# Optimization experiments

Hardware: AMD Instinct MI355X
Metric: run time of the kernel (lower is better)

## Reference

```python
import jax, jax.numpy as jnp
from jax import lax
import numpy as np

E = 256        # encoded_part_size
H = 1500       # builder_hidden_dim == construction_plan_size
QIN = 2 * E    # query_in_size
Q1, Q = 600, 300
EV1, EV2, EV3, EV4 = 1000, 100, 10, 1
B, N = 32, 32  # batch, parts


def _lin(key, fan_in, shape):
    b = 1.0 / np.sqrt(fan_in)
    return jax.random.uniform(key, shape, jnp.float32, -b, b)


def setup_inputs() -> dict:
    key = jax.random.key(0)
    ks = jax.random.split(key, 20)
    inp = {"x": jax.random.normal(ks[0], (B, N, E), jnp.float32)}
    # LSTMCell params (torch gate order i,f,g,o)
    inp["w_ih"] = _lin(ks[1], H, (4 * H, E))
    inp["w_hh"] = _lin(ks[2], H, (4 * H, H))
    inp["b_ih"] = _lin(ks[3], H, (4 * H,))
    inp["b_hh"] = _lin(ks[4], H, (4 * H,))
    # query MLP
    inp["q1_w"] = _lin(ks[5], QIN, (Q1, QIN)); inp["q1_b"] = _lin(ks[6], QIN, (Q1,))
    inp["q2_w"] = _lin(ks[7], Q1, (Q, Q1));   inp["q2_b"] = _lin(ks[8], Q1, (Q,))
    # evaluator MLP
    inp["e1_w"] = _lin(ks[9], H + Q, (EV1, H + Q)); inp["e1_b"] = _lin(ks[10], H + Q, (EV1,))
    inp["e2_w"] = _lin(ks[11], EV1, (EV2, EV1));    inp["e2_b"] = _lin(ks[12], EV1, (EV2,))
    inp["e3_w"] = _lin(ks[13], EV2, (EV3, EV2));    inp["e3_b"] = _lin(ks[14], EV2, (EV3,))
    inp["e4_w"] = _lin(ks[15], EV3, (EV4, EV3));    inp["e4_b"] = _lin(ks[16], EV3, (EV4,))
    return inp


def reference(x, w_ih, w_hh, b_ih, b_hh, q1_w, q1_b, q2_w, q2_b,
              e1_w, e1_b, e2_w, e2_b, e3_w, e3_b, e4_w, e4_b):
    b, n, e = x.shape
    h = w_hh.shape[1]

    # ---- makeConstructionPlan: sort parts, run LSTMCell over the sequence ----
    seq = jnp.sort(x, axis=1).transpose(1, 0, 2)  # [n, B, E]

    def step(carry, xt):
        hs, cs = carry
        g = xt @ w_ih.T + b_ih + hs @ w_hh.T + b_hh  # [B, 4H]
        gi, gf, gg, go = jnp.split(g, 4, axis=-1)
        cs = jax.nn.sigmoid(gf) * cs + jax.nn.sigmoid(gi) * jnp.tanh(gg)
        hs = jax.nn.sigmoid(go) * jnp.tanh(cs)
        return (hs, cs), None

    z = jnp.zeros((b, h), x.dtype)
    (plan, _), _ = lax.scan(step, (z, z), seq)  # plan: [B, H]

    # ---- all pairs (i<j), batched instead of O(n^2) Python loop ----
    ii, jj = jnp.triu_indices(n, k=1)                       # P pairs, row-major order
    pairs = jnp.concatenate([x[:, ii], x[:, jj]], axis=-1)  # [B, P, 2E]

    # PositionalEncoding at position 0: sin(0)=0 on even dims, cos(0)=1 on odd dims
    pe = jnp.zeros((2 * e,), x.dtype).at[1::2].set(1.0)
    q = jax.nn.relu((pairs + pe) @ q1_w.T + q1_b)
    q = jax.nn.relu(q @ q2_w.T + q2_b)                      # [B, P, Qs]

    # evaluator: split the concat GEMM so the [B,P,H+Q] concat is never materialized
    ev = jax.nn.relu((plan @ e1_w[:, :h].T + e1_b)[:, None, :] + q @ e1_w[:, h:].T)
    ev = jax.nn.relu(ev @ e2_w.T + e2_b)
    ev = jax.nn.relu(ev @ e3_w.T + e3_b)
    ev = jax.nn.relu(ev @ e4_w.T + e4_b)                    # [B, P, 1]
    return ev[..., 0]                                       # [B, P]
```

## Files before the change

kernel.cpp:

```cpp
#include <hip/hip_runtime.h>
#include <math.h>

#define BB 32
#define NN 32
#define EE 256
#define HH 1500
#define G4 6000
#define QIN 512
#define Q1O 600
#define QO 300
#define EV1 1000
#define EV2 100
#define EV3 10
#define PP 496
#define ROWS (BB*PP)
#define BH (BB*HH)

#define TROW 40
#define TPLANE (128 * TROW)

#define LKT 47
#define LBLK 375
#define LTILE 1024
#define HSZ (LKT * LTILE)
#define LTILE_W 512
#define HSZW (LKT * LTILE_W)

typedef __attribute__((ext_vector_type(8))) short bf16x8;
typedef __attribute__((ext_vector_type(4))) float f32x4;

__device__ __forceinline__ float sigm(float x) { return 1.f / (1.f + expf(-x)); }

__device__ __forceinline__ unsigned bf16h(float x) {
    unsigned u = __float_as_uint(x);
    return (u + 0x7FFFu + ((u >> 16) & 1u)) & 0xFFFF0000u;
}

__device__ __forceinline__ void split4(float4 v, short* hp, short* lp) {
    unsigned h0 = bf16h(v.x), h1 = bf16h(v.y), h2 = bf16h(v.z), h3 = bf16h(v.w);
    float r0 = v.x - __uint_as_float(h0);
    float r1 = v.y - __uint_as_float(h1);
    float r2 = v.z - __uint_as_float(h2);
    float r3 = v.w - __uint_as_float(h3);
    unsigned l0 = bf16h(r0), l1 = bf16h(r1), l2 = bf16h(r2), l3 = bf16h(r3);
    uint2 hw, lw;
    hw.x = (h0 >> 16) | (h1 & 0xFFFF0000u);
    hw.y = (h2 >> 16) | (h3 & 0xFFFF0000u);
    lw.x = (l0 >> 16) | (l1 & 0xFFFF0000u);
    lw.y = (l2 >> 16) | (l3 & 0xFFFF0000u);
    *(uint2*)hp = hw;
    *(uint2*)lp = lw;
}

__device__ __forceinline__ void hi4(float4 v, short* hp) {
    unsigned h0 = bf16h(v.x), h1 = bf16h(v.y), h2 = bf16h(v.z), h3 = bf16h(v.w);
    uint2 hw;
    hw.x = (h0 >> 16) | (h1 & 0xFFFF0000u);
    hw.y = (h2 >> 16) | (h3 & 0xFFFF0000u);
    *(uint2*)hp = hw;
}

#define ASYNC16(dst, src) \
    __builtin_amdgcn_global_load_lds((const __attribute__((address_space(1))) unsigned*)(src), \
                                     (__attribute__((address_space(3))) unsigned*)(dst), 16, 0, 0)

__global__ void k_zero(float* a, int n) {
    int i = blockIdx.x * 256 + threadIdx.x;
    if (i < n) a[i] = 0.f;
}

__global__ void k_iijj(int* iijj) {
    int p = threadIdx.x;
    if (p >= PP) return;
    int i = 0, p0 = 0;
    while (p >= p0 + (NN - 1 - i)) { p0 += NN - 1 - i; i++; }
    iijj[p] = i;
    iijj[PP + p] = i + 1 + (p - p0);
}

__global__ void k_q1beff(const float* q1w, const float* q1b, float* beff) {
    int o = blockIdx.x * 256 + threadIdx.x;
    if (o >= Q1O) return;
    float a = q1b[o];
    for (int k = 1; k < QIN; k += 2) a += q1w[o * QIN + k];
    beff[o] = a;
}

__global__ void k_addb(const float* a, const float* b, float* c, int n) {
    int i = blockIdx.x * 256 + threadIdx.x;
    if (i < n) c[i] = a[i] + b[i];
}

__global__ void k_transpose(const float* __restrict__ src, float* __restrict__ dst,
                            int R, int C, int c0, int csub) {
    __shared__ float tile[32][33];
    int cb = blockIdx.x * 32, rb = blockIdx.y * 32;
    for (int dy = threadIdx.y; dy < 32; dy += 8) {
        int r = rb + dy, c = cb + threadIdx.x;
        if (r < R && c < csub) tile[dy][threadIdx.x] = src[(size_t)r * C + c0 + c];
    }
    __syncthreads();
    for (int dy = threadIdx.y; dy < 32; dy += 8) {
        int c = cb + dy, r = rb + threadIdx.x;
        if (c < csub && r < R) dst[(size_t)c * R + r] = tile[threadIdx.x][dy];
    }
}

__global__ void k_pack(const float* __restrict__ src, int ld, int col0, int NR, int K,
                       short* __restrict__ D) {
    int kt = blockIdx.x, mt = blockIdx.y, KT = gridDim.x;
    size_t tb = ((size_t)mt * KT + kt) * (2 * TPLANE);
    for (int idx = threadIdx.x; idx < 1024; idx += 256) {
        int rowin = idx >> 3, k4 = (idx & 7) << 2;
        int r = mt * 128 + rowin, k = kt * 32 + k4;
        float4 v = {0.f, 0.f, 0.f, 0.f};
        if (r < NR && k < K) v = *(const float4*)(src + (size_t)r * ld + col0 + k);
        size_t o = tb + rowin * TROW + k4;
        split4(v, D + o, D + o + TPLANE);
    }
}

__global__ void k_pack1(const float* __restrict__ src, int ld, int col0, int NR, int K,
                        short* __restrict__ D) {
    int kt = blockIdx.x, mt = blockIdx.y, KT = gridDim.x;
    size_t tb = ((size_t)mt * KT + kt) * TPLANE;
    for (int idx = threadIdx.x; idx < 1024; idx += 256) {
        int rowin = idx >> 3, k4 = (idx & 7) << 2;
        int r = mt * 128 + rowin, k = kt * 32 + k4;
        float4 v = {0.f, 0.f, 0.f, 0.f};
        if (r < NR && k < K) v = *(const float4*)(src + (size_t)r * ld + col0 + k);
        hi4(v, D + tb + rowin * TROW + k4);
    }
}

__global__ void k_pack_wf(const float* __restrict__ whh, short* __restrict__ wf) {
    int kt = blockIdx.x, blk = blockIdx.y;
    size_t tb = ((size_t)blk * LKT + kt) * LTILE_W;
    int t = threadIdx.x;
    int row = t >> 3, k4 = (t & 7) << 2;
    int g = row & 3, h_glob = blk * 4 + (row >> 2);
    int k = kt * 32 + k4;
    float4 v = {0.f, 0.f, 0.f, 0.f};
    if (k < HH) {
        int j = g * HH + h_glob;
        v = *(const float4*)(whh + (size_t)j * HH + k);
    }
    hi4(v, wf + tb + row * 32 + k4);
}

__global__ void k_sort(const float* __restrict__ x, float* __restrict__ seq) {
    int tid = blockIdx.x * 256 + threadIdx.x;
    if (tid >= BB * EE) return;
    int b = tid / EE, e = tid % EE;
    float v[NN];
#pragma unroll
    for (int n = 0; n < NN; n++) v[n] = x[(b * NN + n) * EE + e];
#pragma unroll
    for (int kk = 2; kk <= NN; kk <<= 1) {
#pragma unroll
        for (int jj = kk >> 1; jj > 0; jj >>= 1) {
#pragma unroll
            for (int i = 0; i < NN; i++) {
                int l = i ^ jj;
                if (l > i) {
                    bool up = (i & kk) == 0;
                    float a = v[i], c = v[l];
                    bool sw = up ? (a > c) : (a < c);
                    float lo = sw ? c : a, hi = sw ? a : c;
                    v[i] = lo; v[l] = hi;
                }
            }
        }
    }
#pragma unroll
    for (int n = 0; n < NN; n++) seq[(n * BB + b) * EE + e] = v[n];
}

__global__ void k_pairs(const float* __restrict__ x, const int* __restrict__ iijj,
                        short* __restrict__ P) {
    int idx = blockIdx.x * 256 + threadIdx.x;
    int r = idx >> 7;
    if (r >= ROWS) return;
    int q = idx & 127, k = q << 2;
    int b = r / PP, p = r - b * PP;
    int part = (k < EE) ? iijj[p] : iijj[PP + p];
    float4 v = *(const float4*)(x + (size_t)(b * NN + part) * EE + (k & (EE - 1)));
    int mt = r >> 7, rowin = r & 127, kt = k >> 5, k4 = k & 31;
    size_t o = ((size_t)mt * 16 + kt) * TPLANE + rowin * TROW + k4;
    hi4(v, P + o);
}

template<int APL, int BPL, int PPL>
__global__ __launch_bounds__(256, 2)
void k_gemm_t(const short* __restrict__ Ap, int AKT, const short* __restrict__ Bp,
              const float* __restrict__ bias, const float* __restrict__ pbm,
              float* __restrict__ Cf32, short* __restrict__ P, int PKT,
              int M, int K, int N, int relu, int cmode) {
    const int ATS = APL * TPLANE;
    const int BTS = BPL * TPLANE;
    constexpr bool PIPE = (APL == 1 && BPL == 1);
    constexpr int DEPTH = PIPE ? 3 : 2;
    __shared__ __align__(16) short lds[DEPTH][(APL + BPL) * TPLANE];

    int MT = M >> 7, NT = (N + 127) >> 7;
    int bid = blockIdx.x;
    int xcd = bid & 7, rr = bid >> 3;
    int nt = rr % NT, mtc = rr / NT;
    int mt = mtc * 8 + xcd;
    if (mt >= MT) return;

    int tid = threadIdx.x;
    int lane = tid & 63, w = tid >> 6;
    int wr = w >> 1, wc = w & 1;
    int ksteps = (K + 31) >> 5;

    const short* gA = Ap + (size_t)mt * AKT * ATS;
    const short* gB = Bp + (size_t)nt * ksteps * BTS;

    f32x4 acc[4][4];
#pragma unroll
    for (int mi = 0; mi < 4; mi++)
#pragma unroll
        for (int ni = 0; ni < 4; ni++) acc[mi][ni] = (f32x4){0.f, 0.f, 0.f, 0.f};

    int l15 = lane & 15;
    int kc8 = (lane >> 4) << 3;

    if constexpr (PIPE) {
#define STAGE3(bufi, kt) do { \
            _Pragma("unroll") \
            for (int i_ = 0; i_ < 5; i_++) { \
                int c_ = w * 5 + i_; \
                const short* s_ = (c_ < 10) \
                    ? gA + (size_t)(kt) * ATS + (c_ << 9) + lane * 8 \
                    : gB + (size_t)(kt) * BTS + ((c_ - 10) << 9) + lane * 8; \
                ASYNC16(&lds[bufi][c_ << 9], s_); \
            } \
        } while (0)

        STAGE3(0, 0);
        if (ksteps > 1) STAGE3(1, 1);

        int cbuf = 0, sbuf = 2;
        for (int kt = 0; kt < ksteps; kt++) {
            if (kt + 1 < ksteps) asm volatile("s_waitcnt vmcnt(5)" ::: "memory");
            else                 asm volatile("s_waitcnt vmcnt(0)" ::: "memory");
            __builtin_amdgcn_s_barrier();

            const short* LA = &lds[cbuf][0];
            const short* LB = &lds[cbuf][TPLANE];
            bf16x8 ah[4];
#pragma unroll
            for (int mi = 0; mi < 4; mi++)
                ah[mi] = *(const bf16x8*)(LA + (wr * 64 + mi * 16 + l15) * TROW + kc8);
#pragma unroll
            for (int ni = 0; ni < 4; ni++) {
                bf16x8 bh = *(const bf16x8*)(LB + (wc * 64 + ni * 16 + l15) * TROW + kc8);
#pragma unroll
                for (int mi = 0; mi < 4; mi++)
                    acc[mi][ni] = __builtin_amdgcn_mfma_f32_16x16x32_bf16(ah[mi], bh, acc[mi][ni], 0, 0, 0);
            }
            if (kt + 2 < ksteps) STAGE3(sbuf, kt + 2);
            cbuf = (cbuf == 2) ? 0 : cbuf + 1;
            sbuf = (sbuf == 2) ? 0 : sbuf + 1;
        }
#undef STAGE3
    } else {
#define STAGE(bufi, kt) do { \
            const short* sa_ = gA + (size_t)(kt) * ATS + lane * 8; \
            const short* sb_ = gB + (size_t)(kt) * BTS + lane * 8; \
            for (int c_ = w; c_ < ATS / 512; c_ += 4) \
                ASYNC16(&lds[bufi][c_ * 512], sa_ + c_ * 512); \
            for (int c_ = w; c_ < BTS / 512; c_ += 4) \
                ASYNC16(&lds[bufi][ATS + c_ * 512], sb_ + c_ * 512); \
        } while (0)

        STAGE(0, 0);
        __syncthreads();
        int buf = 0;
        for (int kt = 0; kt < ksteps; kt++) {
            if (kt + 1 < ksteps) STAGE(buf ^ 1, kt + 1);
            const short* LA = &lds[buf][0];
            const short* LB = &lds[buf][ATS];
            bf16x8 ah[4], al[4];
#pragma unroll
            for (int mi = 0; mi < 4; mi++) {
                int o = (wr * 64 + mi * 16 + l15) * TROW + kc8;
                ah[mi] = *(const bf16x8*)(LA + o);
                if constexpr (APL == 2) al[mi] = *(const bf16x8*)(LA + TPLANE + o);
            }
#pragma unroll
            for (int ni = 0; ni < 4; ni++) {
                int o = (wc * 64 + ni * 16 + l15) * TROW + kc8;
                bf16x8 bh = *(const bf16x8*)(LB + o);
                bf16x8 bl;
                if constexpr (BPL == 2) bl = *(const bf16x8*)(LB + TPLANE + o);
#pragma unroll
                for (int mi = 0; mi < 4; mi++) {
                    acc[mi][ni] = __builtin_amdgcn_mfma_f32_16x16x32_bf16(ah[mi], bh, acc[mi][ni], 0, 0, 0);
                    if constexpr (BPL == 2)
                        acc[mi][ni] = __builtin_amdgcn_mfma_f32_16x16x32_bf16(ah[mi], bl, acc[mi][ni], 0, 0, 0);
                    if constexpr (APL == 2)
                        acc[mi][ni] = __builtin_amdgcn_mfma_f32_16x16x32_bf16(al[mi], bh, acc[mi][ni], 0, 0, 0);
                }
            }
            __syncthreads();
            buf ^= 1;
        }
#undef STAGE
    }

    const int PTS = PPL * TPLANE;
#pragma unroll
    for (int ni = 0; ni < 4; ni++) {
        int col = nt * 128 + wc * 64 + ni * 16 + l15;
        float bb = (cmode == 0 && bias && col < N) ? bias[col] : 0.f;
#pragma unroll
        for (int mi = 0; mi < 4; mi++) {
            int rbase = mt * 128 + wr * 64 + mi * 16 + ((lane >> 4) << 2);
#pragma unroll
            for (int r4 = 0; r4 < 4; r4++) {
                int row = rbase + r4;
                float v = acc[mi][ni][r4];
                if (cmode == 1) {
                    if (row < G4)
                        Cf32[(size_t)(col >> 5) * (G4 * BB) + (size_t)row * BB + (col & 31)]
                            = v + bias[row];
                    continue;
                }
                v += bb;
                if (pbm && col < N) v += pbm[(size_t)(row / PP) * N + col];
                if (relu) v = fmaxf(v, 0.f);
                if (Cf32 && col < N) Cf32[(size_t)row * N + col] = v;
                if (P) {
                    unsigned h = bf16h(v);
                    int kt2 = col >> 5, kin = col & 31, rowin = row & 127, mtt = row >> 7;
                    size_t o = ((size_t)mtt * PKT + kt2) * PTS + rowin * TROW + kin;
                    P[o] = (short)(h >> 16);
                    if constexpr (PPL == 2) {
                        unsigned l = bf16h(v - __uint_as_float(h));
                        P[o + TPLANE] = (short)(l >> 16);
                    }
                }
            }
        }
    }
}

__global__ __launch_bounds__(512, 1)
void k_lstm_step(const short* __restrict__ wf, const short* __restrict__ hbuf_r,
                 short* __restrict__ hbuf_w, const float* __restrict__ xgT_n,
                 float* __restrict__ ct, float* __restrict__ ht, int writeht) {
    __shared__ f32x4 red[3][2][64];
    int tid = threadIdx.x, lane = tid & 63, wave = tid >> 6;
    int ks = wave >> 1, mi = wave & 1;
    int blk = blockIdx.x;
    int l15 = lane & 15, bg = lane >> 4;
    int kc8 = bg << 3;
    int n = l15, g = n & 3;
    int h_glob = blk * 4 + (n >> 2);
    int kt0 = ks * 12, ktend = (ks == 3) ? LKT : (kt0 + 12);

    f32x4 acc = {0.f, 0.f, 0.f, 0.f};
    if (ks == 0)
        acc = *(const f32x4*)(xgT_n + (size_t)(g * HH + h_glob) * BB + mi * 16 + bg * 4);

    const short* wp0 = wf + (size_t)blk * HSZW + l15 * 32 + kc8;
    const short* hp0 = hbuf_r + (mi * 16 + l15) * 32 + kc8;

    bf16x8 a0 = *(const bf16x8*)(hp0 + (size_t)kt0 * LTILE);
    bf16x8 b0 = *(const bf16x8*)(wp0 + (size_t)kt0 * LTILE_W);
    bf16x8 a1 = *(const bf16x8*)(hp0 + (size_t)(kt0 + 1) * LTILE);
    bf16x8 b1 = *(const bf16x8*)(wp0 + (size_t)(kt0 + 1) * LTILE_W);
    bf16x8 a2 = *(const bf16x8*)(hp0 + (size_t)(kt0 + 2) * LTILE);
    bf16x8 b2 = *(const bf16x8*)(wp0 + (size_t)(kt0 + 2) * LTILE_W);
    for (int kt = kt0; kt < ktend; kt++) {
        bf16x8 a3, b3;
        if (kt + 3 < ktend) {
            a3 = *(const bf16x8*)(hp0 + (size_t)(kt + 3) * LTILE);
            b3 = *(const bf16x8*)(wp0 + (size_t)(kt + 3) * LTILE_W);
        }
        acc = __builtin_amdgcn_mfma_f32_16x16x32_bf16(a0, b0, acc, 0, 0, 0);
        a0 = a1; b0 = b1;
        a1 = a2; b1 = b2;
        a2 = a3; b2 = b3;
    }

    if (ks > 0) red[ks - 1][mi][lane] = acc;
    __syncthreads();
    if (ks > 0) return;
    acc += red[0][mi][lane] + red[1][mi][lane] + red[2][mi][lane];

    float gg[4][4];
#pragma unroll
    for (int r = 0; r < 4; r++) {
        float a = acc[r];
        gg[0][r] = a;
        gg[1][r] = __shfl_xor(a, 1);
        gg[2][r] = __shfl_xor(a, 2);
        gg[3][r] = __shfl_xor(a, 3);
    }

    if ((n & 3) == 0) {
        int kth = h_glob >> 5, kin = h_glob & 31;
#pragma unroll
        for (int r = 0; r < 4; r++) {
            int b = mi * 16 + bg * 4 + r;
            float ci = ct[h_glob * BB + b];
            float cn = sigm(gg[1][r]) * ci + sigm(gg[0][r]) * tanhf(gg[2][r]);
            ct[h_glob * BB + b] = cn;
            float hv = sigm(gg[3][r]) * tanhf(cn);
            if (writeht) ht[h_glob * BB + b] = hv;
            unsigned hh = bf16h(hv);
            size_t o = (size_t)kth * LTILE + b * 32 + kin;
            __builtin_nontemporal_store((short)(hh >> 16), &hbuf_w[o]);
        }
    }
}

__global__ void k_pb(const float* __restrict__ ht, const float* __restrict__ e1at,
                     const float* __restrict__ e1b, float* __restrict__ pb) {
    __shared__ float ps[HH];
    int b = blockIdx.y;
    for (int idx = threadIdx.x; idx < HH; idx += 256) ps[idx] = ht[(size_t)idx * BB + b];
    __syncthreads();
    int o = blockIdx.x * 256 + threadIdx.x;
    if (o >= EV1) return;
    float acc = e1b[o];
    for (int k = 0; k < HH; k++) acc += ps[k] * e1at[(size_t)k * EV1 + o];
    pb[b * EV1 + o] = acc;
}

__global__ void k_e34(const float* __restrict__ e2out, const float* __restrict__ e3t,
                      const float* __restrict__ e3b, const float* __restrict__ e4w,
                      const float* __restrict__ e4b, float* __restrict__ out) {
    __shared__ float wt[EV2 * EV3];
    for (int idx = threadIdx.x; idx < EV2 * EV3; idx += 256) wt[idx] = e3t[idx];
    __syncthreads();
    int r = blockIdx.x * 256 + threadIdx.x;
    if (r >= ROWS) return;
    float h3[EV3];
#pragma unroll
    for (int o3 = 0; o3 < EV3; o3++) h3[o3] = e3b[o3];
    for (int k = 0; k < EV2; k++) {
        float v = e2out[(size_t)r * EV2 + k];
#pragma unroll
        for (int o3 = 0; o3 < EV3; o3++) h3[o3] += v * wt[k * EV3 + o3];
    }
    float acc = e4b[0];
#pragma unroll
    for (int o3 = 0; o3 < EV3; o3++) acc += fmaxf(h3[o3], 0.f) * e4w[o3];
    out[r] = fmaxf(acc, 0.f);
}

extern "C" void kernel_launch(void* const* d_in, const int* in_sizes, int n_in,
                              void* d_out, int out_size, void* d_ws, size_t ws_size,
                              hipStream_t stream) {
    const float* x    = (const float*)d_in[0];
    const float* w_ih = (const float*)d_in[1];
    const float* w_hh = (const float*)d_in[2];
    const float* b_ih = (const float*)d_in[3];
    const float* b_hh = (const float*)d_in[4];
    const float* q1_w = (const float*)d_in[5];
    const float* q1_b = (const float*)d_in[6];
    const float* q2_w = (const float*)d_in[7];
    const float* q2_b = (const float*)d_in[8];
    const float* e1_w = (const float*)d_in[9];
    const float* e1_b = (const float*)d_in[10];
    const float* e2_w = (const float*)d_in[11];
    const float* e2_b = (const float*)d_in[12];
    const float* e3_w = (const float*)d_in[13];
    const float* e3_b = (const float*)d_in[14];
    const float* e4_w = (const float*)d_in[15];
    const float* e4_b = (const float*)d_in[16];
    float* out = (float*)d_out;
    float* ws = (float*)d_ws;

    size_t off = 0;
    float* seq    = ws + off; off += (size_t)NN * BB * EE;
    size_t regionA = off; off += 23000000;
    short* wf       = (short*)(ws + regionA);
    short* seq_p    = (short*)(ws + regionA + 4600000);
    short* wih_p    = (short*)(ws + regionA + 5000000);
    short* pairs_p  = (short*)(ws + regionA);
    short* q1out_p  = (short*)(ws + regionA + 10200000);
    short* e1out_p  = (short*)(ws + regionA);
    float* e2out    = ws + regionA + 20400000;
    float* xgT    = ws + off; off += 7618560;
    short* q2out_p  = (short*)xgT;
    float* ht     = ws + off; off += BH;
    float* ct     = ws + off; off += BH;
    short* hbuf   = (short*)(ws + off); off += 48128;
    short* q1w_p  = (short*)(ws + off); off += 409600;
    short* q2w_p  = (short*)(ws + off); off += 291840;
    short* e1w_p  = (short*)(ws + off); off += 409600;
    short* e2w_p  = (short*)(ws + off); off += 163840;
    float* e1at   = ws + off; off += (size_t)HH * EV1;
    float* e3t    = ws + off; off += 1024;
    float* pb     = ws + off; off += BB * EV1;
    float* q1beff = ws + off; off += 1024;
    float* bsum   = ws + off; off += 6016;
    int*   iijj   = (int*)(ws + off); off += 1024;

    dim3 tb(32, 8);

    k_iijj<<<1, 512, 0, stream>>>(iijj);
    k_q1beff<<<3, 256, 0, stream>>>(q1_w, q1_b, q1beff);
    k_addb<<<24, 256, 0, stream>>>(b_ih, b_hh, bsum, G4);
    k_zero<<<376, 256, 0, stream>>>(ct, BH + 48128);

    k_pack_wf<<<dim3(LKT, LBLK), 128, 0, stream>>>(w_hh, wf);
    k_transpose<<<dim3(47, 32), tb, 0, stream>>>(e1_w, e1at, EV1, HH + QO, 0, HH);
    k_transpose<<<dim3(4, 1), tb, 0, stream>>>(e3_w, e3t, EV3, EV2, 0, EV2);
    k_pack<<<dim3(8, 47), 256, 0, stream>>>(w_ih, EE, 0, G4, EE, wih_p);
    k_pack1<<<dim3(16, 5), 256, 0, stream>>>(q1_w, QIN, 0, Q1O, QIN, q1w_p);
    k_pack1<<<dim3(19, 3), 256, 0, stream>>>(q2_w, Q1O, 0, QO, Q1O, q2w_p);
    k_pack1<<<dim3(10, 8), 256, 0, stream>>>(e1_w, HH + QO, HH, EV1, QO, e1w_p);
    k_pack1<<<dim3(32, 1), 256, 0, stream>>>(e2_w, EV1, 0, EV2, EV1, e2w_p);

    k_sort<<<32, 256, 0, stream>>>(x, seq);
    k_pack<<<dim3(8, 8), 256, 0, stream>>>(seq, EE, 0, 1024, EE, seq_p);
    k_gemm_t<2, 2, 1><<<8 * 8 * 6, 256, 0, stream>>>(wih_p, 8, seq_p, bsum, nullptr,
                                                     xgT, nullptr, 0, 6016, EE, 1024, 0, 1);

    for (int nstep = 0; nstep < NN; nstep++) {
        const short* hr = hbuf + (size_t)(nstep & 1) * HSZ;
        short* hw = hbuf + (size_t)((nstep + 1) & 1) * HSZ;
        k_lstm_step<<<LBLK, 512, 0, stream>>>(wf, hr, hw,
                                              xgT + (size_t)nstep * (G4 * BB), ct, ht,
                                              nstep == NN - 1);
    }

    k_pb<<<dim3(4, BB), 256, 0, stream>>>(ht, e1at, e1_b, pb);

    k_pairs<<<7936, 256, 0, stream>>>(x, iijj, pairs_p);
    k_gemm_t<1, 1, 1><<<8 * 5 * 16, 256, 0, stream>>>(pairs_p, 16, q1w_p, q1beff, nullptr,
                                                      nullptr, q1out_p, 20, ROWS, QIN, Q1O, 1, 0);
    k_gemm_t<1, 1, 1><<<8 * 3 * 16, 256, 0, stream>>>(q1out_p, 20, q2w_p, q2_b, nullptr,
                                                      nullptr, q2out_p, 12, ROWS, Q1O, QO, 1, 0);
    k_gemm_t<1, 1, 1><<<8 * 8 * 16, 256, 0, stream>>>(q2out_p, 12, e1w_p, nullptr, pb,
                                                      nullptr, e1out_p, 32, ROWS, QO, EV1, 1, 0);
    k_gemm_t<1, 1, 1><<<8 * 1 * 16, 256, 0, stream>>>(e1out_p, 32, e2w_p, e2_b, nullptr,
                                                      e2out, nullptr, 0, ROWS, EV1, EV2, 1, 0);
    k_e34<<<62, 256, 0, stream>>>(e2out, e3t, e3_b, e4_w, e4_b, out);
}
```

Baseline: 766.7 us.

## Deepen GEMM async pipeline to four stages and stage bf16 epilogue through LDS

The pipelined GEMM now uses four LDS buffers with three k-tiles prefetched, and the vmcnt waits are adjusted to how many loads are still in flight. The packed-bf16 output epilogue is also rewritten for the pipelined variant. It writes results into LDS tiles, loads the per-batch bias rows once into LDS, and copies whole tiles to global memory with 16-byte stores instead of scattered 2-byte stores. The cost is more LDS per block, which may lower occupancy under launch_bounds(256,2), plus extra barriers in the epilogue.

```diff
diff --git a/kernel.cpp b/kernel.cpp
--- a/kernel.cpp
+++ b/kernel.cpp
@@ -199,7 +199,7 @@
     const int ATS = APL * TPLANE;
     const int BTS = BPL * TPLANE;
     constexpr bool PIPE = (APL == 1 && BPL == 1);
-    constexpr int DEPTH = PIPE ? 3 : 2;
+    constexpr int DEPTH = PIPE ? 4 : 2;
     __shared__ __align__(16) short lds[DEPTH][(APL + BPL) * TPLANE];
 
     int MT = M >> 7, NT = (N + 127) >> 7;
@@ -240,15 +240,17 @@
 
         STAGE3(0, 0);
         if (ksteps > 1) STAGE3(1, 1);
-
-        int cbuf = 0, sbuf = 2;
+        if (ksteps > 2) STAGE3(2, 2);
+
         for (int kt = 0; kt < ksteps; kt++) {
-            if (kt + 1 < ksteps) asm volatile("s_waitcnt vmcnt(5)" ::: "memory");
+            int ahead = ksteps - 1 - kt;
+            if (ahead >= 2)      asm volatile("s_waitcnt vmcnt(10)" ::: "memory");
+            else if (ahead == 1) asm volatile("s_waitcnt vmcnt(5)" ::: "memory");
             else                 asm volatile("s_waitcnt vmcnt(0)" ::: "memory");
             __builtin_amdgcn_s_barrier();
 
-            const short* LA = &lds[cbuf][0];
-            const short* LB = &lds[cbuf][TPLANE];
+            const short* LA = &lds[kt & 3][0];
+            const short* LB = &lds[kt & 3][TPLANE];
             bf16x8 ah[4];
 #pragma unroll
             for (int mi = 0; mi < 4; mi++)
@@ -260,9 +262,7 @@
                 for (int mi = 0; mi < 4; mi++)
                     acc[mi][ni] = __builtin_amdgcn_mfma_f32_16x16x32_bf16(ah[mi], bh, acc[mi][ni], 0, 0, 0);
             }
-            if (kt + 2 < ksteps) STAGE3(sbuf, kt + 2);
-            cbuf = (cbuf == 2) ? 0 : cbuf + 1;
-            sbuf = (sbuf == 2) ? 0 : sbuf + 1;
+            if (kt + 3 < ksteps) STAGE3((kt + 3) & 3, kt + 3);
         }
 #undef STAGE3
     } else {
@@ -310,36 +310,90 @@
 #undef STAGE
     }
 
-    const int PTS = PPL * TPLANE;
-#pragma unroll
-    for (int ni = 0; ni < 4; ni++) {
-        int col = nt * 128 + wc * 64 + ni * 16 + l15;
-        float bb = (cmode == 0 && bias && col < N) ? bias[col] : 0.f;
-#pragma unroll
-        for (int mi = 0; mi < 4; mi++) {
-            int rbase = mt * 128 + wr * 64 + mi * 16 + ((lane >> 4) << 2);
-#pragma unroll
-            for (int r4 = 0; r4 < 4; r4++) {
-                int row = rbase + r4;
-                float v = acc[mi][ni][r4];
-                if (cmode == 1) {
-                    if (row < G4)
-                        Cf32[(size_t)(col >> 5) * (G4 * BB) + (size_t)row * BB + (col & 31)]
-                            = v + bias[row];
-                    continue;
+    bool done = false;
+    if constexpr (PIPE) {
+        if (P) {
+            short* obuf = &lds[0][0];
+            float* pbv  = (float*)&lds[1][0];
+            int b0 = (mt * 128) / PP;
+            int thr = (b0 + 1) * PP;
+            __syncthreads();
+            if (pbm) {
+                int c = nt * 128 + (tid & 127);
+                int bsel = (tid < 128) ? b0 : min(b0 + 1, BB - 1);
+                pbv[tid] = (c < N) ? pbm[(size_t)bsel * N + c] : 0.f;
+            }
+            __syncthreads();
+            int bg = lane >> 4;
+#pragma unroll
+            for (int r = 0; r < 2; r++) {
+#pragma unroll
+                for (int p = 0; p < 2; p++) {
+                    int ni = 2 * r + p;
+                    int col = nt * 128 + wc * 64 + ni * 16 + l15;
+                    int colloc = wc * 64 + ni * 16 + l15;
+                    float bb = (bias && col < N) ? bias[col] : 0.f;
+                    int kin = p * 16 + l15;
+#pragma unroll
+                    for (int mi = 0; mi < 4; mi++) {
+#pragma unroll
+                        for (int r4 = 0; r4 < 4; r4++) {
+                            int rowin = wr * 64 + mi * 16 + (bg << 2) + r4;
+                            float v = acc[mi][ni][r4] + bb;
+                            if (pbm) {
+                                int row = mt * 128 + rowin;
+                                v += pbv[(row >= thr ? 128 : 0) + colloc];
+                            }
+                            if (relu) v = fmaxf(v, 0.f);
+                            obuf[wc * 5120 + rowin * 40 + kin] = (short)(bf16h(v) >> 16);
+                        }
+                    }
                 }
-                v += bb;
-                if (pbm && col < N) v += pbm[(size_t)(row / PP) * N + col];
-                if (relu) v = fmaxf(v, 0.f);
-                if (Cf32 && col < N) Cf32[(size_t)row * N + col] = v;
-                if (P) {
-                    unsigned h = bf16h(v);
-                    int kt2 = col >> 5, kin = col & 31, rowin = row & 127, mtt = row >> 7;
-                    size_t o = ((size_t)mtt * PKT + kt2) * PTS + rowin * TROW + kin;
-                    P[o] = (short)(h >> 16);
-                    if constexpr (PPL == 2) {
-                        unsigned l = bf16h(v - __uint_as_float(h));
-                        P[o + TPLANE] = (short)(l >> 16);
+                __syncthreads();
+#pragma unroll
+                for (int reg = 0; reg < 2; reg++) {
+                    int ktg = nt * 4 + reg * 2 + r;
+                    uint4* dst = (uint4*)(P + ((size_t)mt * PKT + ktg) * TPLANE);
+                    const uint4* srcl = (const uint4*)(obuf + reg * 5120);
+                    for (int c = tid; c < 640; c += 256) dst[c] = srcl[c];
+                }
+                __syncthreads();
+            }
+            done = true;
+        }
+    }
+    if (!done) {
+        const int PTS = PPL * TPLANE;
+#pragma unroll
+        for (int ni = 0; ni < 4; ni++) {
+            int col = nt * 128 + wc * 64 + ni * 16 + l15;
+            float bb = (cmode == 0 && bias && col < N) ? bias[col] : 0.f;
+#pragma unroll
+            for (int mi = 0; mi < 4; mi++) {
+                int rbase = mt * 128 + wr * 64 + mi * 16 + ((lane >> 4) << 2);
+#pragma unroll
+                for (int r4 = 0; r4 < 4; r4++) {
+                    int row = rbase + r4;
+                    float v = acc[mi][ni][r4];
+                    if (cmode == 1) {
+                        if (row < G4)
+                            Cf32[(size_t)(col >> 5) * (G4 * BB) + (size_t)row * BB + (col & 31)]
+                                = v + bias[row];
+                        continue;
+                    }
+                    v += bb;
+                    if (pbm && col < N) v += pbm[(size_t)(row / PP) * N + col];
+                    if (relu) v = fmaxf(v, 0.f);
+                    if (Cf32 && col < N) Cf32[(size_t)row * N + col] = v;
+                    if (P) {
+                        unsigned h = bf16h(v);
+                        int kt2 = col >> 5, kin = col & 31, rowin = row & 127, mtt = row >> 7;
+                        size_t o = ((size_t)mtt * PKT + kt2) * PTS + rowin * TROW + kin;
+                        P[o] = (short)(h >> 16);
+                        if constexpr (PPL == 2) {
+                            unsigned l = bf16h(v - __uint_as_float(h));
+                            P[o + TPLANE] = (short)(l >> 16);
+                        }
                     }
                 }
             }
```

After: 708.1 us. 7.6% less time.
